# Kernel optimization log

Hardware: AMD Instinct MI355X
Metric: run time of the kernel (lower is better)

## Reference

```python
import jax, jax.numpy as jnp
import numpy as np

ALPHA = 0.2  # LeakyReLU negative slope
MASK_VAL = -1e12


def setup_inputs() -> dict:
    key = jax.random.key(0)
    k1, k2, k3, k4 = jax.random.split(key, 4)
    B, N, F_in, F_out = 16, 1024, 128, 64
    inp = jax.random.normal(k1, (B, N, F_in), dtype=jnp.float32)
    adj = jax.random.randint(k2, (B, N, N), 0, 2, dtype=jnp.int32)
    W = jax.random.normal(k3, (F_in, F_out), dtype=jnp.float32) * (1.414 / np.sqrt(F_in))
    a = jax.random.normal(k4, (2 * F_out, 1), dtype=jnp.float32) * (1.414 / np.sqrt(2 * F_out))
    return {"inp": inp, "adj": adj, "W": W, "a": a}


def reference(inp, adj, W, a):
    # inp: [B, N, F_in], adj: [B, N, N], W: [F_in, F_out], a: [2*F_out, 1]
    F_out = W.shape[1]
    h = jnp.einsum('bnf,fo->bno', inp, W)  # [B, N, F_out]
    # e_ij = LeakyReLU(a1 . h_i + a2 . h_j)  (equivalent to concat-then-matmul)
    a1 = a[:F_out, 0]  # [F_out]
    a2 = a[F_out:, 0]  # [F_out]
    e = jax.nn.leaky_relu(
        (h @ a1)[:, :, None] + (h @ a2)[:, None, :], negative_slope=ALPHA
    )  # [B, N, N]
    scores = jnp.where(adj > 0, e, MASK_VAL)
    attention = jax.nn.softmax(scores, axis=-1)  # [B, N, N]
    # dropout with p=0.0 / eval mode -> identity
    h_prime = jnp.einsum('bij,bjo->bio', attention, h)  # [B, N, F_out]
    return jax.nn.elu(h_prime)  # concat=True
```

## Files before the change

kernel.cpp:

```cpp
#include <hip/hip_runtime.h>
#include <cstdint>

#define BB   16
#define NN   1024
#define FIN  128
#define FOUT 64
#define ALPHA_S 0.2f
#define LOG2E 1.44269504f

typedef float    f32x4 __attribute__((ext_vector_type(4)));
typedef _Float16 half8 __attribute__((ext_vector_type(8)));
typedef _Float16 half4 __attribute__((ext_vector_type(4)));
typedef __fp16   pk2   __attribute__((ext_vector_type(2)));
typedef __fp16   pk4   __attribute__((ext_vector_type(4)));
typedef __fp16   pk8   __attribute__((ext_vector_type(8)));

__device__ __forceinline__ float fast_exp2(float x){
  float r; asm("v_exp_f32 %0, %1" : "=v"(r) : "v"(x)); return r;
}

__global__ __launch_bounds__(256) void k_proj(const float* __restrict__ inp,
                                              const float* __restrict__ W,
                                              const float* __restrict__ a,
                                              _Float16* __restrict__ hT,
                                              float* __restrict__ s1,
                                              float* __restrict__ s2){
  __shared__ float red1[4][16];
  __shared__ float red2[4][16];
  const int t = threadIdx.x;
  const int w = t >> 6, lane = t & 63;
  const int m16 = lane & 15, g = lane >> 4;
  const int i0 = blockIdx.x * 16;
  const int b  = i0 >> 10;
  const int j0 = i0 & 1023;
  const int c0 = w * 16;

  const float* arow = inp + (size_t)(i0 + m16) * FIN;

  f32x4 acc = {0.f, 0.f, 0.f, 0.f};
  #pragma unroll
  for (int kk = 0; kk < 4; ++kk){
    const int kbase = kk * 32 + g * 8;
    float4 av0 = *(const float4*)(arow + kbase);
    float4 av1 = *(const float4*)(arow + kbase + 4);
    const float av[8] = {av0.x, av0.y, av0.z, av0.w, av1.x, av1.y, av1.z, av1.w};
    half8 ah, al;
    #pragma unroll
    for (int j = 0; j < 8; ++j){
      _Float16 h = (_Float16)av[j];
      ah[j] = h;
      al[j] = (_Float16)(av[j] - (float)h);
    }
    half8 bh, bl;
    #pragma unroll
    for (int j = 0; j < 8; ++j){
      float wv = W[(kbase + j) * FOUT + c0 + m16];
      _Float16 h = (_Float16)wv;
      bh[j] = h;
      bl[j] = (_Float16)(wv - (float)h);
    }
    acc = __builtin_amdgcn_mfma_f32_16x16x32_f16(ah, bh, acc, 0, 0, 0);
    acc = __builtin_amdgcn_mfma_f32_16x16x32_f16(ah, bl, acc, 0, 0, 0);
    acc = __builtin_amdgcn_mfma_f32_16x16x32_f16(al, bh, acc, 0, 0, 0);
  }

  const float a1c = a[c0 + m16];
  const float a2c = a[FOUT + c0 + m16];
  f32x4 p1, p2;
  #pragma unroll
  for (int q = 0; q < 4; ++q){ p1[q] = acc[q] * a1c; p2[q] = acc[q] * a2c; }
  #pragma unroll
  for (int off = 1; off < 16; off <<= 1){
    #pragma unroll
    for (int q = 0; q < 4; ++q){
      p1[q] += __shfl_xor(p1[q], off, 64);
      p2[q] += __shfl_xor(p2[q], off, 64);
    }
  }
  if (m16 == 0){
    #pragma unroll
    for (int q = 0; q < 4; ++q){
      red1[w][g * 4 + q] = p1[q];
      red2[w][g * 4 + q] = p2[q];
    }
  }

  half4 hv;
  #pragma unroll
  for (int q = 0; q < 4; ++q) hv[q] = (_Float16)acc[q];
  size_t idx = (size_t)b * 65536 + (size_t)(j0 >> 5) * 2048
             + (size_t)(c0 + m16) * 32 + (size_t)(j0 & 31) + (size_t)g * 4;
  *(half4*)(hT + idx) = hv;

  __syncthreads();
  if (t < 16){
    s1[i0 + t] = (red1[0][t] + red1[1][t] + red1[2][t] + red1[3][t]) * LOG2E;
    s2[i0 + t] = (red2[0][t] + red2[1][t] + red2[2][t] + red2[3][t]) * LOG2E;
  }
}

__global__ __launch_bounds__(256) void k_attn(const int* __restrict__ adj,
                                              const _Float16* __restrict__ hT,
                                              const float* __restrict__ s1,
                                              const float* __restrict__ s2,
                                              float* __restrict__ out){
  __shared__ float s2_s[NN];
  __shared__ float redmax[4][16];
  __shared__ float redl[4][16];
  __shared__ float csum[4][1088];

  const int t = threadIdx.x;
  const int w = t >> 6, lane = t & 63;
  const int m16 = lane & 15, g = lane >> 4;
  const int b  = blockIdx.x >> 6;
  const int i0 = (blockIdx.x & 63) * 16;
  const int jb = w * 256;

  *(float4*)&s2_s[jb + lane * 4] = *(const float4*)(s2 + b * NN + jb + lane * 4);

  const int* arow = adj + ((size_t)(b * NN + i0 + m16)) * NN + jb + g * 8;
  int4 A0[8], A1[8];
  #pragma unroll
  for (int kk = 0; kk < 8; ++kk){
    A0[kk] = *(const int4*)(arow + kk * 32);
    A1[kk] = *(const int4*)(arow + kk * 32 + 4);
  }

  const float s1i = s1[b * NN + i0 + m16];

  float sm[64];
  float mxp = -3.0e38f;
  #pragma unroll
  for (int kk = 0; kk < 8; ++kk){
    float4 sA = *(const float4*)&s2_s[jb + kk * 32 + g * 8];
    float4 sB = *(const float4*)&s2_s[jb + kk * 32 + g * 8 + 4];
    float v;
    v = (A0[kk].x > 0) ? sA.x : -3.0e38f; sm[kk*8+0] = v; mxp = fmaxf(mxp, v);
    v = (A0[kk].y > 0) ? sA.y : -3.0e38f; sm[kk*8+1] = v; mxp = fmaxf(mxp, v);
    v = (A0[kk].z > 0) ? sA.z : -3.0e38f; sm[kk*8+2] = v; mxp = fmaxf(mxp, v);
    v = (A0[kk].w > 0) ? sA.w : -3.0e38f; sm[kk*8+3] = v; mxp = fmaxf(mxp, v);
    v = (A1[kk].x > 0) ? sB.x : -3.0e38f; sm[kk*8+4] = v; mxp = fmaxf(mxp, v);
    v = (A1[kk].y > 0) ? sB.y : -3.0e38f; sm[kk*8+5] = v; mxp = fmaxf(mxp, v);
    v = (A1[kk].z > 0) ? sB.z : -3.0e38f; sm[kk*8+6] = v; mxp = fmaxf(mxp, v);
    v = (A1[kk].w > 0) ? sB.w : -3.0e38f; sm[kk*8+7] = v; mxp = fmaxf(mxp, v);
  }

  mxp = fmaxf(mxp, __shfl_xor(mxp, 16, 64));
  mxp = fmaxf(mxp, __shfl_xor(mxp, 32, 64));
  mxp = fmaxf(mxp, -1.0e30f);
  const float xm   = s1i + mxp;
  const float mrow = fmaxf(xm, ALPHA_S * xm);
  if (g == 0) redmax[w][m16] = mrow;
  const float s1m = s1i - mrow;
  const float c2  = ALPHA_S * s1i - mrow;

  f32x4 acc0 = {0,0,0,0}, acc1 = {0,0,0,0}, acc2 = {0,0,0,0}, acc3 = {0,0,0,0};
  float psA = 0.f, psB = 0.f;
  const size_t bbase = (size_t)b * 65536 + (size_t)(w * 8) * 2048
                     + (size_t)m16 * 32 + (size_t)g * 8;
  const _Float16* bhp = hT + bbase;

  #pragma unroll
  for (int kk = 0; kk < 8; ++kk){
    float p0 = fast_exp2(fmaxf(s1m + sm[kk*8+0], fmaf(ALPHA_S, sm[kk*8+0], c2)));
    float p1 = fast_exp2(fmaxf(s1m + sm[kk*8+1], fmaf(ALPHA_S, sm[kk*8+1], c2)));
    float p2 = fast_exp2(fmaxf(s1m + sm[kk*8+2], fmaf(ALPHA_S, sm[kk*8+2], c2)));
    float p3 = fast_exp2(fmaxf(s1m + sm[kk*8+3], fmaf(ALPHA_S, sm[kk*8+3], c2)));
    float p4 = fast_exp2(fmaxf(s1m + sm[kk*8+4], fmaf(ALPHA_S, sm[kk*8+4], c2)));
    float p5 = fast_exp2(fmaxf(s1m + sm[kk*8+5], fmaf(ALPHA_S, sm[kk*8+5], c2)));
    float p6 = fast_exp2(fmaxf(s1m + sm[kk*8+6], fmaf(ALPHA_S, sm[kk*8+6], c2)));
    float p7 = fast_exp2(fmaxf(s1m + sm[kk*8+7], fmaf(ALPHA_S, sm[kk*8+7], c2)));
    psA += (p0 + p1) + (p2 + p3);
    psB += (p4 + p5) + (p6 + p7);
    pk2 q0 = __builtin_amdgcn_cvt_pkrtz(p0, p1);
    pk2 q1 = __builtin_amdgcn_cvt_pkrtz(p2, p3);
    pk2 q2 = __builtin_amdgcn_cvt_pkrtz(p4, p5);
    pk2 q3 = __builtin_amdgcn_cvt_pkrtz(p6, p7);
    pk4 l0 = __builtin_shufflevector(q0, q1, 0, 1, 2, 3);
    pk4 l1 = __builtin_shufflevector(q2, q3, 0, 1, 2, 3);
    pk8 afp = __builtin_shufflevector(l0, l1, 0, 1, 2, 3, 4, 5, 6, 7);
    half8 af = __builtin_bit_cast(half8, afp);
    half8 b0 = *(const half8*)(bhp + kk * 2048);
    half8 b1 = *(const half8*)(bhp + kk * 2048 + 512);
    half8 b2 = *(const half8*)(bhp + kk * 2048 + 1024);
    half8 b3 = *(const half8*)(bhp + kk * 2048 + 1536);
    acc0 = __builtin_amdgcn_mfma_f32_16x16x32_f16(af, b0, acc0, 0, 0, 0);
    acc1 = __builtin_amdgcn_mfma_f32_16x16x32_f16(af, b1, acc1, 0, 0, 0);
    acc2 = __builtin_amdgcn_mfma_f32_16x16x32_f16(af, b2, acc2, 0, 0, 0);
    acc3 = __builtin_amdgcn_mfma_f32_16x16x32_f16(af, b3, acc3, 0, 0, 0);
  }

  float psum = psA + psB;
  psum += __shfl_xor(psum, 16, 64);
  psum += __shfl_xor(psum, 32, 64);
  if (g == 0) redl[w][m16] = psum;

  #pragma unroll
  for (int q = 0; q < 4; ++q){
    csum[w][(g * 4 + q) * 68 +  0 + m16] = acc0[q];
    csum[w][(g * 4 + q) * 68 + 16 + m16] = acc1[q];
    csum[w][(g * 4 + q) * 68 + 32 + m16] = acc2[q];
    csum[w][(g * 4 + q) * 68 + 48 + m16] = acc3[q];
  }
  __syncthreads();

  const int r  = t >> 4;
  const int c4 = (t & 15) * 4;
  const float m0 = redmax[0][r], m1 = redmax[1][r];
  const float m2 = redmax[2][r], m3 = redmax[3][r];
  const float mg = fmaxf(fmaxf(m0, m1), fmaxf(m2, m3));
  const float f0 = fast_exp2(m0 - mg), f1 = fast_exp2(m1 - mg);
  const float f2 = fast_exp2(m2 - mg), f3 = fast_exp2(m3 - mg);

  f32x4 c0v = *(const f32x4*)&csum[0][r * 68 + c4];
  f32x4 c1v = *(const f32x4*)&csum[1][r * 68 + c4];
  f32x4 c2v = *(const f32x4*)&csum[2][r * 68 + c4];
  f32x4 c3v = *(const f32x4*)&csum[3][r * 68 + c4];
  f32x4 sum;
  #pragma unroll
  for (int u = 0; u < 4; ++u)
    sum[u] = c0v[u] * f0 + c1v[u] * f1 + c2v[u] * f2 + c3v[u] * f3;

  const float l = redl[0][r] * f0 + redl[1][r] * f1
                + redl[2][r] * f2 + redl[3][r] * f3;
  const float linv = (l > 0.f) ? __builtin_amdgcn_rcpf(l) : 0.f;
  f32x4 o;
  #pragma unroll
  for (int u = 0; u < 4; ++u){
    float v = sum[u] * linv;
    o[u] = v > 0.f ? v : __expf(v) - 1.0f;
  }
  *(f32x4*)(out + ((size_t)(b * NN + i0 + r)) * FOUT + c4) = o;
}

extern "C" void kernel_launch(void* const* d_in, const int* in_sizes, int n_in,
                              void* d_out, int out_size, void* d_ws, size_t ws_size,
                              hipStream_t stream) {
  (void)in_sizes; (void)n_in; (void)out_size; (void)ws_size;
  const float* inp = (const float*)d_in[0];
  const int*   adj = (const int*)d_in[1];
  const float* W   = (const float*)d_in[2];
  const float* a   = (const float*)d_in[3];
  float* outp = (float*)d_out;

  _Float16* hT = (_Float16*)d_ws;
  float* s1 = (float*)(hT + (size_t)BB * 65536);
  float* s2 = s1 + BB * NN;

  k_proj<<<BB * NN / 16, 256, 0, stream>>>(inp, W, a, hT, s1, s2);
  k_attn<<<BB * (NN / 16), 256, 0, stream>>>(adj, hT, s1, s2, outp);
}
```

Measured before the change: 116.5 us.

## Stream adjacency in chunks with online softmax rescaling to cut register pressure

The attention kernel stops preloading all 64 adjacency ints per lane and the full masked-score array. It now processes four 64-column chunks, double-buffering adjacency loads and keeping an online running max, rescaling the partial sums and MFMA accumulators whenever the max grows. s2 is read straight from global memory instead of being staged in shared memory, and launch bounds request 4 blocks per SM to raise occupancy. The trade is fewer live registers against extra exp2 and rescale work and cross-lane shuffles for each chunk.

```diff
diff --git a/kernel.cpp b/kernel.cpp
--- a/kernel.cpp
+++ b/kernel.cpp
@@ -99,12 +99,11 @@
   }
 }
 
-__global__ __launch_bounds__(256) void k_attn(const int* __restrict__ adj,
-                                              const _Float16* __restrict__ hT,
-                                              const float* __restrict__ s1,
-                                              const float* __restrict__ s2,
-                                              float* __restrict__ out){
-  __shared__ float s2_s[NN];
+__global__ __launch_bounds__(256, 4) void k_attn(const int* __restrict__ adj,
+                                                 const _Float16* __restrict__ hT,
+                                                 const float* __restrict__ s1,
+                                                 const float* __restrict__ s2,
+                                                 float* __restrict__ out){
   __shared__ float redmax[4][16];
   __shared__ float redl[4][16];
   __shared__ float csum[4][1088];
@@ -116,80 +115,125 @@
   const int i0 = (blockIdx.x & 63) * 16;
   const int jb = w * 256;
 
-  *(float4*)&s2_s[jb + lane * 4] = *(const float4*)(s2 + b * NN + jb + lane * 4);
-
-  const int* arow = adj + ((size_t)(b * NN + i0 + m16)) * NN + jb + g * 8;
-  int4 A0[8], A1[8];
-  #pragma unroll
-  for (int kk = 0; kk < 8; ++kk){
-    A0[kk] = *(const int4*)(arow + kk * 32);
-    A1[kk] = *(const int4*)(arow + kk * 32 + 4);
-  }
-
-  const float s1i = s1[b * NN + i0 + m16];
-
-  float sm[64];
-  float mxp = -3.0e38f;
-  #pragma unroll
-  for (int kk = 0; kk < 8; ++kk){
-    float4 sA = *(const float4*)&s2_s[jb + kk * 32 + g * 8];
-    float4 sB = *(const float4*)&s2_s[jb + kk * 32 + g * 8 + 4];
-    float v;
-    v = (A0[kk].x > 0) ? sA.x : -3.0e38f; sm[kk*8+0] = v; mxp = fmaxf(mxp, v);
-    v = (A0[kk].y > 0) ? sA.y : -3.0e38f; sm[kk*8+1] = v; mxp = fmaxf(mxp, v);
-    v = (A0[kk].z > 0) ? sA.z : -3.0e38f; sm[kk*8+2] = v; mxp = fmaxf(mxp, v);
-    v = (A0[kk].w > 0) ? sA.w : -3.0e38f; sm[kk*8+3] = v; mxp = fmaxf(mxp, v);
-    v = (A1[kk].x > 0) ? sB.x : -3.0e38f; sm[kk*8+4] = v; mxp = fmaxf(mxp, v);
-    v = (A1[kk].y > 0) ? sB.y : -3.0e38f; sm[kk*8+5] = v; mxp = fmaxf(mxp, v);
-    v = (A1[kk].z > 0) ? sB.z : -3.0e38f; sm[kk*8+6] = v; mxp = fmaxf(mxp, v);
-    v = (A1[kk].w > 0) ? sB.w : -3.0e38f; sm[kk*8+7] = v; mxp = fmaxf(mxp, v);
-  }
-
-  mxp = fmaxf(mxp, __shfl_xor(mxp, 16, 64));
-  mxp = fmaxf(mxp, __shfl_xor(mxp, 32, 64));
-  mxp = fmaxf(mxp, -1.0e30f);
-  const float xm   = s1i + mxp;
-  const float mrow = fmaxf(xm, ALPHA_S * xm);
-  if (g == 0) redmax[w][m16] = mrow;
-  const float s1m = s1i - mrow;
-  const float c2  = ALPHA_S * s1i - mrow;
+  const int*   arow = adj + ((size_t)(b * NN + i0 + m16)) * NN + jb + g * 8;
+  const float* s2p  = s2 + b * NN + jb + g * 8;
+  const float  s1i  = s1[b * NN + i0 + m16];
+  const _Float16* bhp = hT + (size_t)b * 65536 + (size_t)(w * 8) * 2048
+                      + (size_t)m16 * 32 + (size_t)g * 8;
+
+  int4 Abuf[2][4];
+  Abuf[0][0] = *(const int4*)(arow + 0);
+  Abuf[0][1] = *(const int4*)(arow + 4);
+  Abuf[0][2] = *(const int4*)(arow + 32);
+  Abuf[0][3] = *(const int4*)(arow + 36);
 
   f32x4 acc0 = {0,0,0,0}, acc1 = {0,0,0,0}, acc2 = {0,0,0,0}, acc3 = {0,0,0,0};
   float psA = 0.f, psB = 0.f;
-  const size_t bbase = (size_t)b * 65536 + (size_t)(w * 8) * 2048
-                     + (size_t)m16 * 32 + (size_t)g * 8;
-  const _Float16* bhp = hT + bbase;
-
-  #pragma unroll
-  for (int kk = 0; kk < 8; ++kk){
-    float p0 = fast_exp2(fmaxf(s1m + sm[kk*8+0], fmaf(ALPHA_S, sm[kk*8+0], c2)));
-    float p1 = fast_exp2(fmaxf(s1m + sm[kk*8+1], fmaf(ALPHA_S, sm[kk*8+1], c2)));
-    float p2 = fast_exp2(fmaxf(s1m + sm[kk*8+2], fmaf(ALPHA_S, sm[kk*8+2], c2)));
-    float p3 = fast_exp2(fmaxf(s1m + sm[kk*8+3], fmaf(ALPHA_S, sm[kk*8+3], c2)));
-    float p4 = fast_exp2(fmaxf(s1m + sm[kk*8+4], fmaf(ALPHA_S, sm[kk*8+4], c2)));
-    float p5 = fast_exp2(fmaxf(s1m + sm[kk*8+5], fmaf(ALPHA_S, sm[kk*8+5], c2)));
-    float p6 = fast_exp2(fmaxf(s1m + sm[kk*8+6], fmaf(ALPHA_S, sm[kk*8+6], c2)));
-    float p7 = fast_exp2(fmaxf(s1m + sm[kk*8+7], fmaf(ALPHA_S, sm[kk*8+7], c2)));
-    psA += (p0 + p1) + (p2 + p3);
-    psB += (p4 + p5) + (p6 + p7);
-    pk2 q0 = __builtin_amdgcn_cvt_pkrtz(p0, p1);
-    pk2 q1 = __builtin_amdgcn_cvt_pkrtz(p2, p3);
-    pk2 q2 = __builtin_amdgcn_cvt_pkrtz(p4, p5);
-    pk2 q3 = __builtin_amdgcn_cvt_pkrtz(p6, p7);
+  float mold = -3.0e38f;
+
+  #pragma unroll
+  for (int cc = 0; cc < 4; ++cc){
+    const int ph = cc & 1;
+    if (cc < 3){
+      const int np = ph ^ 1;
+      const int nb = (cc + 1) * 64;
+      Abuf[np][0] = *(const int4*)(arow + nb);
+      Abuf[np][1] = *(const int4*)(arow + nb + 4);
+      Abuf[np][2] = *(const int4*)(arow + nb + 32);
+      Abuf[np][3] = *(const int4*)(arow + nb + 36);
+    }
+    const int cb = cc * 64;
+    const float4 S0 = *(const float4*)(s2p + cb);
+    const float4 S1 = *(const float4*)(s2p + cb + 4);
+    const float4 S2 = *(const float4*)(s2p + cb + 32);
+    const float4 S3 = *(const float4*)(s2p + cb + 36);
+
+    float smv[16];
+    float cmax = -3.0e38f;
+    {
+      const int4 Av0 = Abuf[ph][0], Av1 = Abuf[ph][1];
+      const int4 Av2 = Abuf[ph][2], Av3 = Abuf[ph][3];
+      float v;
+      v = (Av0.x > 0) ? S0.x : -3.0e38f; smv[ 0] = v; cmax = fmaxf(cmax, v);
+      v = (Av0.y > 0) ? S0.y : -3.0e38f; smv[ 1] = v; cmax = fmaxf(cmax, v);
+      v = (Av0.z > 0) ? S0.z : -3.0e38f; smv[ 2] = v; cmax = fmaxf(cmax, v);
+      v = (Av0.w > 0) ? S0.w : -3.0e38f; smv[ 3] = v; cmax = fmaxf(cmax, v);
+      v = (Av1.x > 0) ? S1.x : -3.0e38f; smv[ 4] = v; cmax = fmaxf(cmax, v);
+      v = (Av1.y > 0) ? S1.y : -3.0e38f; smv[ 5] = v; cmax = fmaxf(cmax, v);
+      v = (Av1.z > 0) ? S1.z : -3.0e38f; smv[ 6] = v; cmax = fmaxf(cmax, v);
+      v = (Av1.w > 0) ? S1.w : -3.0e38f; smv[ 7] = v; cmax = fmaxf(cmax, v);
+      v = (Av2.x > 0) ? S2.x : -3.0e38f; smv[ 8] = v; cmax = fmaxf(cmax, v);
+      v = (Av2.y > 0) ? S2.y : -3.0e38f; smv[ 9] = v; cmax = fmaxf(cmax, v);
+      v = (Av2.z > 0) ? S2.z : -3.0e38f; smv[10] = v; cmax = fmaxf(cmax, v);
+      v = (Av2.w > 0) ? S2.w : -3.0e38f; smv[11] = v; cmax = fmaxf(cmax, v);
+      v = (Av3.x > 0) ? S3.x : -3.0e38f; smv[12] = v; cmax = fmaxf(cmax, v);
+      v = (Av3.y > 0) ? S3.y : -3.0e38f; smv[13] = v; cmax = fmaxf(cmax, v);
+      v = (Av3.z > 0) ? S3.z : -3.0e38f; smv[14] = v; cmax = fmaxf(cmax, v);
+      v = (Av3.w > 0) ? S3.w : -3.0e38f; smv[15] = v; cmax = fmaxf(cmax, v);
+    }
+    cmax = fmaxf(cmax, __shfl_xor(cmax, 16, 64));
+    cmax = fmaxf(cmax, __shfl_xor(cmax, 32, 64));
+    const float xm   = s1i + cmax;
+    const float mc   = fmaxf(xm, ALPHA_S * xm);
+    const float mnew = fmaxf(mold, mc);
+    if (cc){
+      const float frv = fast_exp2(mold - mnew);
+      psA *= frv; psB *= frv;
+      #pragma unroll
+      for (int q = 0; q < 4; ++q){
+        const float frq = __shfl(frv, g * 4 + q, 64);
+        acc0[q] *= frq; acc1[q] *= frq; acc2[q] *= frq; acc3[q] *= frq;
+      }
+    }
+    mold = mnew;
+    const float s1m = s1i - mnew;
+    const float c2  = ALPHA_S * s1i - mnew;
+
+    float p[16];
+    #pragma unroll
+    for (int u = 0; u < 16; ++u)
+      p[u] = fast_exp2(fmaxf(s1m + smv[u], fmaf(ALPHA_S, smv[u], c2)));
+    psA += ((p[0] + p[1]) + (p[2] + p[3])) + ((p[4] + p[5]) + (p[6] + p[7]));
+    psB += ((p[8] + p[9]) + (p[10] + p[11])) + ((p[12] + p[13]) + (p[14] + p[15]));
+
+    pk2 q0 = __builtin_amdgcn_cvt_pkrtz(p[ 0], p[ 1]);
+    pk2 q1 = __builtin_amdgcn_cvt_pkrtz(p[ 2], p[ 3]);
+    pk2 q2 = __builtin_amdgcn_cvt_pkrtz(p[ 4], p[ 5]);
+    pk2 q3 = __builtin_amdgcn_cvt_pkrtz(p[ 6], p[ 7]);
+    pk2 q4 = __builtin_amdgcn_cvt_pkrtz(p[ 8], p[ 9]);
+    pk2 q5 = __builtin_amdgcn_cvt_pkrtz(p[10], p[11]);
+    pk2 q6 = __builtin_amdgcn_cvt_pkrtz(p[12], p[13]);
+    pk2 q7 = __builtin_amdgcn_cvt_pkrtz(p[14], p[15]);
     pk4 l0 = __builtin_shufflevector(q0, q1, 0, 1, 2, 3);
     pk4 l1 = __builtin_shufflevector(q2, q3, 0, 1, 2, 3);
-    pk8 afp = __builtin_shufflevector(l0, l1, 0, 1, 2, 3, 4, 5, 6, 7);
-    half8 af = __builtin_bit_cast(half8, afp);
-    half8 b0 = *(const half8*)(bhp + kk * 2048);
-    half8 b1 = *(const half8*)(bhp + kk * 2048 + 512);
-    half8 b2 = *(const half8*)(bhp + kk * 2048 + 1024);
-    half8 b3 = *(const half8*)(bhp + kk * 2048 + 1536);
-    acc0 = __builtin_amdgcn_mfma_f32_16x16x32_f16(af, b0, acc0, 0, 0, 0);
-    acc1 = __builtin_amdgcn_mfma_f32_16x16x32_f16(af, b1, acc1, 0, 0, 0);
-    acc2 = __builtin_amdgcn_mfma_f32_16x16x32_f16(af, b2, acc2, 0, 0, 0);
-    acc3 = __builtin_amdgcn_mfma_f32_16x16x32_f16(af, b3, acc3, 0, 0, 0);
-  }
-
+    pk4 l2 = __builtin_shufflevector(q4, q5, 0, 1, 2, 3);
+    pk4 l3 = __builtin_shufflevector(q6, q7, 0, 1, 2, 3);
+    half8 af0 = __builtin_bit_cast(half8,
+                  __builtin_shufflevector(l0, l1, 0, 1, 2, 3, 4, 5, 6, 7));
+    half8 af1 = __builtin_bit_cast(half8,
+                  __builtin_shufflevector(l2, l3, 0, 1, 2, 3, 4, 5, 6, 7));
+
+    const _Float16* bp0 = bhp + (size_t)(cc * 2) * 2048;
+    const _Float16* bp1 = bp0 + 2048;
+    half8 b00 = *(const half8*)(bp0);
+    half8 b01 = *(const half8*)(bp0 + 512);
+    half8 b02 = *(const half8*)(bp0 + 1024);
+    half8 b03 = *(const half8*)(bp0 + 1536);
+    half8 b10 = *(const half8*)(bp1);
+    half8 b11 = *(const half8*)(bp1 + 512);
+    half8 b12 = *(const half8*)(bp1 + 1024);
+    half8 b13 = *(const half8*)(bp1 + 1536);
+    acc0 = __builtin_amdgcn_mfma_f32_16x16x32_f16(af0, b00, acc0, 0, 0, 0);
+    acc1 = __builtin_amdgcn_mfma_f32_16x16x32_f16(af0, b01, acc1, 0, 0, 0);
+    acc2 = __builtin_amdgcn_mfma_f32_16x16x32_f16(af0, b02, acc2, 0, 0, 0);
+    acc3 = __builtin_amdgcn_mfma_f32_16x16x32_f16(af0, b03, acc3, 0, 0, 0);
+    acc0 = __builtin_amdgcn_mfma_f32_16x16x32_f16(af1, b10, acc0, 0, 0, 0);
+    acc1 = __builtin_amdgcn_mfma_f32_16x16x32_f16(af1, b11, acc1, 0, 0, 0);
+    acc2 = __builtin_amdgcn_mfma_f32_16x16x32_f16(af1, b12, acc2, 0, 0, 0);
+    acc3 = __builtin_amdgcn_mfma_f32_16x16x32_f16(af1, b13, acc3, 0, 0, 0);
+  }
+
+  if (g == 0) redmax[w][m16] = mold;
   float psum = psA + psB;
   psum += __shfl_xor(psum, 16, 64);
   psum += __shfl_xor(psum, 32, 64);
```

New measurement: 125.5 us. +7.7%, slower.
